# Kernel tuning notes

Measured on AMD Instinct MI355X. Metric: run time of the kernel, lower is better.

Reference implementation:

```python
import jax, jax.numpy as jnp
import numpy as np

NUM_CLASSES = 200
MARGIN = 0.6
LAMBDA_WEIGHT = 0.2
ALPHA = 1.5
GAMMA = 0.8
EPS = 1e-8


def setup_inputs() -> dict:
    key = jax.random.key(0)
    k1, k2 = jax.random.split(key)
    B, D = 32768, 512
    features = jax.random.normal(k1, (B, D), dtype=jnp.float32)
    labels = jax.random.randint(k2, (B,), 0, NUM_CLASSES, dtype=jnp.int64)
    return {"features": features, "labels": labels}


def reference(features, labels):
    B, D = features.shape
    C = NUM_CLASSES
    labels = labels.astype(jnp.int32)

    # Per-class prototypes (segment mean), matching mask-sum / (count + eps)
    proto_sum = jax.ops.segment_sum(features, labels, num_segments=C)      # [C, D]
    counts = jax.ops.segment_sum(jnp.ones((B,), features.dtype), labels, num_segments=C)
    prototypes = proto_sum / (counts[:, None] + EPS)                       # [C, D]

    # Squared distances from every sample to every prototype via Gram trick
    f2 = jnp.sum(features * features, axis=1, keepdims=True)               # [B, 1]
    p2 = jnp.sum(prototypes * prototypes, axis=1)                          # [C]
    d2 = jnp.maximum(f2 + p2[None, :] - 2.0 * features @ prototypes.T, 0.0)  # [B, C]

    # Nearest negative prototype: mask out the positive class with +inf
    pos_mask = jnp.arange(C)[None, :] == labels[:, None]                   # [B, C]
    neg_idx = jnp.argmin(jnp.where(pos_mask, jnp.inf, d2), axis=1)         # [B]

    # Exact squared distances to positive / chosen negative prototypes
    pos_proto = prototypes[labels]                                         # [B, D]
    neg_proto = prototypes[neg_idx]                                        # [B, D]
    d_ap = jnp.sum((features - pos_proto) ** 2, axis=1)                    # [B]
    d_an = jnp.sum((features - neg_proto) ** 2, axis=1)                    # [B]

    # Replicate the original's sequential normalization (d_ap is updated first)
    d_ap_n = d_ap / (d_ap + d_an + EPS)
    d_an_n = d_an / (d_ap_n + d_an + EPS)

    per_sample = jnp.maximum(0.0, ALPHA * d_ap_n - GAMMA * d_an_n + MARGIN)
    contrastive_loss = jnp.mean(per_sample)
    return jnp.abs(LAMBDA_WEIGHT * contrastive_loss)
```

## Files before the change

kernel.cpp:

```cpp
#include <hip/hip_runtime.h>
#include <hip/hip_bf16.h>

#define NCLS 200
#define NPADP 224
#define NTW 7
#define DIM 512
#define NSAMP 32768
#define NSEG 8
#define CAP 32
#define BM 64
#define BK 32
#define KIT 16
#define BSTR 40

typedef __attribute__((ext_vector_type(4))) float f32x4;
typedef __attribute__((ext_vector_type(4))) int   i32x4;
typedef __attribute__((ext_vector_type(8))) short bf16x8;

__device__ inline short bf16s(float x) {
  __hip_bfloat16 h = __float2bfloat16(x);
  return *reinterpret_cast<short*>(&h);
}

__device__ inline bf16x8 pack8(f32x4 a, f32x4 b) {
  bf16x8 r;
  r[0] = bf16s(a[0]); r[1] = bf16s(a[1]); r[2] = bf16s(a[2]); r[3] = bf16s(a[3]);
  r[4] = bf16s(b[0]); r[5] = bf16s(b[1]); r[6] = bf16s(b[2]); r[7] = bf16s(b[3]);
  return r;
}

__device__ inline float sumsq(f32x4 a) {
  return a[0]*a[0] + a[1]*a[1] + a[2]*a[2] + a[3]*a[3];
}

__device__ inline void bar_lgkm() {
  asm volatile("s_waitcnt lgkmcnt(0)" ::: "memory");
  __builtin_amdgcn_s_barrier();
}

__global__ __launch_bounds__(512) void k_psum(
    const float* __restrict__ feat, const int* __restrict__ labels,
    float* __restrict__ psum, int* __restrict__ pcnt)
{
  const int bx = blockIdx.x;
  const int c = bx >> 3, s = bx & 7;
  const int tid = threadIdx.x;
  const int lane = tid & 63;
  const int w = tid >> 6;

  __shared__ int   lists[8][CAP];
  __shared__ int   cnts[8];
  __shared__ float partial[8][DIM];

  int cnt = 0;
  const int segbase = s * (NSAMP / NSEG) + w * (NSAMP / NSEG / 8);
  #pragma unroll
  for (int i = 0; i < 2; ++i) {
    const int base = segbase + i * 256 + lane * 4;
    const i32x4 lab4 = *(const i32x4*)(labels + base);
    #pragma unroll
    for (int u = 0; u < 4; ++u) {
      const bool m = (lab4[u] == c);
      const unsigned long long bal = __ballot(m);
      if (m) {
        const int pos = cnt + __popcll(bal & ((1ull << lane) - 1ull));
        if (pos < CAP) lists[w][pos] = base + u;
      }
      cnt += __popcll(bal);
    }
  }
  if (cnt > CAP) cnt = CAP;
  if (lane == 0) cnts[w] = cnt;

  float aE[8], aO[8];
  #pragma unroll
  for (int q = 0; q < 8; ++q) { aE[q] = 0.f; aO[q] = 0.f; }
  int j = 0;
  for (; j + 2 <= cnt; j += 2) {
    const int r0 = lists[w][j], r1 = lists[w][j + 1];
    const f32x4 a0 = *(const f32x4*)(feat + (size_t)r0 * DIM + lane * 8);
    const f32x4 b0 = *(const f32x4*)(feat + (size_t)r0 * DIM + lane * 8 + 4);
    const f32x4 a1 = *(const f32x4*)(feat + (size_t)r1 * DIM + lane * 8);
    const f32x4 b1 = *(const f32x4*)(feat + (size_t)r1 * DIM + lane * 8 + 4);
    aE[0] += a0[0]; aE[1] += a0[1]; aE[2] += a0[2]; aE[3] += a0[3];
    aE[4] += b0[0]; aE[5] += b0[1]; aE[6] += b0[2]; aE[7] += b0[3];
    aO[0] += a1[0]; aO[1] += a1[1]; aO[2] += a1[2]; aO[3] += a1[3];
    aO[4] += b1[0]; aO[5] += b1[1]; aO[6] += b1[2]; aO[7] += b1[3];
  }
  if (j < cnt) {
    const int r0 = lists[w][j];
    const f32x4 a0 = *(const f32x4*)(feat + (size_t)r0 * DIM + lane * 8);
    const f32x4 b0 = *(const f32x4*)(feat + (size_t)r0 * DIM + lane * 8 + 4);
    aE[0] += a0[0]; aE[1] += a0[1]; aE[2] += a0[2]; aE[3] += a0[3];
    aE[4] += b0[0]; aE[5] += b0[1]; aE[6] += b0[2]; aE[7] += b0[3];
  }
  #pragma unroll
  for (int q = 0; q < 8; ++q) partial[w][lane * 8 + q] = aE[q] + aO[q];
  __syncthreads();

  int total = 0;
  #pragma unroll
  for (int u = 0; u < 8; ++u) total += cnts[u];
  float sv = 0.f;
  #pragma unroll
  for (int u = 0; u < 8; ++u) sv += partial[u][tid];
  psum[(size_t)(s * NCLS + c) * DIM + tid] = sv;
  if (tid == 0) pcnt[s * NCLS + c] = total;
}

__global__ __launch_bounds__(256) void k_pcomb(
    const float* __restrict__ psum, const int* __restrict__ pcnt,
    unsigned short* __restrict__ protoI, float* __restrict__ p2out)
{
  const int c = blockIdx.x;
  const int tid = threadIdx.x;
  const int d0 = tid, d1 = tid + 256;
  if (c >= NCLS) {
    protoI[((size_t)(d0 >> 5) * NPADP + c) * 32 + (d0 & 31)] = 0;
    protoI[((size_t)(d1 >> 5) * NPADP + c) * 32 + (d1 & 31)] = 0;
    if (tid == 0) p2out[c] = 1e30f;
    return;
  }
  __shared__ float red[256];
  float a0 = 0.f, a1 = 0.f;
  int total = 0;
  #pragma unroll
  for (int s = 0; s < NSEG; ++s) {
    a0 += psum[(size_t)(s * NCLS + c) * DIM + d0];
    a1 += psum[(size_t)(s * NCLS + c) * DIM + d1];
    total += pcnt[s * NCLS + c];
  }
  const float inv = 1.0f / ((float)total + 1e-8f);
  const float p0 = a0 * inv, p1 = a1 * inv;
  protoI[((size_t)(d0 >> 5) * NPADP + c) * 32 + (d0 & 31)] = (unsigned short)bf16s(p0);
  protoI[((size_t)(d1 >> 5) * NPADP + c) * 32 + (d1 & 31)] = (unsigned short)bf16s(p1);

  red[tid] = p0 * p0 + p1 * p1;
  __syncthreads();
  for (int st = 128; st > 0; st >>= 1) {
    if (tid < st) red[tid] += red[tid + st];
    __syncthreads();
  }
  if (tid == 0) p2out[c] = red[0];
}

__global__ __launch_bounds__(256, 2) void k_score(
    const float* __restrict__ feat, const int* __restrict__ labels,
    const unsigned short* __restrict__ protoI, const float* __restrict__ p2,
    float* __restrict__ partials)
{
  __shared__ __align__(16) unsigned short As[2][BM * BK];
  __shared__ __align__(16) unsigned short Bs[2][NPADP * BSTR];
  __shared__ float f2s[BM][4];
  __shared__ float rd_d[2][BM];
  __shared__ int   rd_c[2][BM];
  __shared__ float rd_p[2][BM];

  const int tid = threadIdx.x;
  const int lane = tid & 63;
  const int w = tid >> 6;
  const int wm = w >> 1, wn = w & 1;
  const int lr = lane & 15;
  const int kg = lane >> 4;
  const int blockRow = blockIdx.x * BM;

  const int arow = tid >> 2, apart = tid & 3;
  const float* agp = feat + (size_t)(blockRow + arow) * DIM + apart * 8;
  const int aoff = arow * BK + ((apart ^ (arow & 3)) * 8);
  const int brow = tid;

#define ISSUE(T, A0, A1, B0, B1, B2, B3) do {                                   \
    const float* ag_ = agp + (T) * BK;                                          \
    A0 = *(const f32x4*)(ag_);                                                  \
    A1 = *(const f32x4*)(ag_ + 4);                                              \
    if (brow < NPADP) {                                                         \
      const f32x4* bg_ = (const f32x4*)(protoI + ((size_t)(T) * NPADP + brow) * 32); \
      B0 = bg_[0]; B1 = bg_[1]; B2 = bg_[2]; B3 = bg_[3];                       \
    }                                                                           \
  } while (0)

#define STORE(NB, A0, A1, B0, B1, B2, B3) do {                                  \
    f2part += sumsq(A0) + sumsq(A1);                                            \
    *(bf16x8*)&As[NB][aoff] = pack8(A0, A1);                                    \
    if (brow < NPADP) {                                                         \
      *(f32x4*)&Bs[NB][brow * BSTR + 0]  = B0;                                  \
      *(f32x4*)&Bs[NB][brow * BSTR + 8]  = B1;                                  \
      *(f32x4*)&Bs[NB][brow * BSTR + 16] = B2;                                  \
      *(f32x4*)&Bs[NB][brow * BSTR + 24] = B3;                                  \
    }                                                                           \
  } while (0)

#define COMPUTE(CUR) do {                                                       \
    const bf16x8 Af0 = *(const bf16x8*)&As[CUR][ar0];                           \
    const bf16x8 Af1 = *(const bf16x8*)&As[CUR][ar1];                           \
    _Pragma("unroll")                                                           \
    for (int n = 0; n < NTW; ++n) {                                             \
      const bf16x8 Bf = *(const bf16x8*)&Bs[CUR][boff + n * (16 * BSTR)];       \
      acc0[n] = __builtin_amdgcn_mfma_f32_16x16x32_bf16(Af0, Bf, acc0[n], 0, 0, 0); \
      acc1[n] = __builtin_amdgcn_mfma_f32_16x16x32_bf16(Af1, Bf, acc1[n], 0, 0, 0); \
    }                                                                           \
  } while (0)

  float f2part = 0.f;
  f32x4 aA0, aA1, bA0, bA1, bA2, bA3;
  f32x4 aB0, aB1, bB0, bB1, bB2, bB3;

  ISSUE(0, aA0, aA1, bA0, bA1, bA2, bA3);
  STORE(0, aA0, aA1, bA0, bA1, bA2, bA3);
  ISSUE(1, aB0, aB1, bB0, bB1, bB2, bB3);
  bar_lgkm();

  f32x4 acc0[NTW], acc1[NTW];
  #pragma unroll
  for (int n = 0; n < NTW; ++n) {
    acc0[n] = f32x4{0.f, 0.f, 0.f, 0.f};
    acc1[n] = f32x4{0.f, 0.f, 0.f, 0.f};
  }

  const int r0v = wm * 32 + lr;
  const int r1v = r0v + 16;
  const int ar0 = r0v * BK + ((kg ^ (r0v & 3)) * 8);
  const int ar1 = r1v * BK + ((kg ^ (r1v & 3)) * 8);
  const int boff = (wn * (NTW * 16) + lr) * BSTR + kg * 8;

  #pragma unroll
  for (int p = 0; p < KIT / 2; ++p) {
    const int t0 = 2 * p, t1 = 2 * p + 1;
    COMPUTE(0);
    if (t0 + 2 < KIT) ISSUE(t0 + 2, aA0, aA1, bA0, bA1, bA2, bA3);
    STORE(1, aB0, aB1, bB0, bB1, bB2, bB3);
    bar_lgkm();
    COMPUTE(1);
    if (t1 + 2 < KIT) {
      ISSUE(t1 + 2, aB0, aB1, bB0, bB1, bB2, bB3);
      STORE(0, aA0, aA1, bA0, bA1, bA2, bA3);
      bar_lgkm();
    }
  }

  f2s[arow][apart] = f2part;
  __syncthreads();

  float p2v[NTW];
  #pragma unroll
  for (int n = 0; n < NTW; ++n) p2v[n] = p2[wn * (NTW * 16) + n * 16 + lr];

  #pragma unroll
  for (int m = 0; m < 2; ++m) {
    #pragma unroll
    for (int r = 0; r < 4; ++r) {
      const int srow = kg * 4 + r;
      const int lrow = wm * 32 + m * 16 + srow;
      const float f2v = (f2s[lrow][0] + f2s[lrow][1]) + (f2s[lrow][2] + f2s[lrow][3]);
      const int lab = labels[blockRow + lrow];
      float bestd = 1e38f; int bestc = 1 << 30;
      float posd = -1.f;
      #pragma unroll
      for (int n = 0; n < NTW; ++n) {
        const int cidx = wn * (NTW * 16) + n * 16 + lr;
        const float sc = (m == 0) ? acc0[n][r] : acc1[n][r];
        const float d2 = fmaxf(f2v + p2v[n] - 2.0f * sc, 0.0f);
        if (cidx == lab) posd = d2;
        else if (cidx < NCLS &&
                 (d2 < bestd || (d2 == bestd && cidx < bestc))) { bestd = d2; bestc = cidx; }
      }
      #pragma unroll
      for (int sft = 1; sft < 16; sft <<= 1) {
        const float od = __shfl_xor(bestd, sft);
        const int   oc = __shfl_xor(bestc, sft);
        const float op = __shfl_xor(posd, sft);
        if (od < bestd || (od == bestd && oc < bestc)) { bestd = od; bestc = oc; }
        posd = fmaxf(posd, op);
      }
      if (lr == 0) {
        rd_d[wn][lrow] = bestd; rd_c[wn][lrow] = bestc; rd_p[wn][lrow] = posd;
      }
    }
  }
  __syncthreads();

  if (tid < BM) {
    const float d0 = rd_d[0][tid], d1 = rd_d[1][tid];
    const int   c0 = rd_c[0][tid], c1 = rd_c[1][tid];
    float bestd; int bestc;
    if (d1 < d0 || (d1 == d0 && c1 < c0)) { bestd = d1; bestc = c1; }
    else                                  { bestd = d0; bestc = c0; }
    (void)bestc;
    const float posd = fmaxf(rd_p[0][tid], rd_p[1][tid]);
    const float dap = posd, dan = bestd;
    const float dapn = dap / (dap + dan + 1e-8f);
    const float dann = dan / (dapn + dan + 1e-8f);
    float v = fmaxf(0.f, 1.5f * dapn - 0.8f * dann + 0.6f);
    #pragma unroll
    for (int sft = 1; sft < 64; sft <<= 1) v += __shfl_xor(v, sft);
    if (tid == 0) partials[blockIdx.x] = v;
  }
#undef ISSUE
#undef STORE
#undef COMPUTE
}

__global__ __launch_bounds__(256) void k_finish(const float* __restrict__ partials,
                                                float* __restrict__ out)
{
  __shared__ float red[256];
  const int tid = threadIdx.x;
  red[tid] = partials[tid] + partials[tid + 256];
  __syncthreads();
  for (int st = 128; st > 0; st >>= 1) {
    if (tid < st) red[tid] += red[tid + st];
    __syncthreads();
  }
  if (tid == 0) out[0] = fabsf(0.2f * (red[0] / (float)NSAMP));
}

extern "C" void kernel_launch(void* const* d_in, const int* in_sizes, int n_in,
                              void* d_out, int out_size, void* d_ws, size_t ws_size,
                              hipStream_t stream) {
  const float* feat = (const float*)d_in[0];
  const int* labels = (const int*)d_in[1];
  float* out = (float*)d_out;

  char* ws = (char*)d_ws;
  unsigned short* protoI = (unsigned short*)ws;
  float* p2 = (float*)(ws + 229376);
  float* partials = (float*)(ws + 230400);
  float* psum = (float*)(ws + 232448);
  int* pcnt = (int*)(ws + 3509248);

  k_psum<<<NSEG * NCLS, 512, 0, stream>>>(feat, labels, psum, pcnt);
  k_pcomb<<<NPADP, 256, 0, stream>>>(psum, pcnt, protoI, p2);
  k_score<<<512, 256, 0, stream>>>(feat, labels, protoI, p2, partials);
  k_finish<<<1, 256, 0, stream>>>(partials, out);
}
```

Before: 46.63 us.

## Load A fragments directly to registers and stage prototypes in 128-wide K chunks

The scoring kernel no longer stages feature rows through shared memory. Each wave loads its A fragments straight from global memory into registers, converts them to bf16 in place, and computes squared norms with cross-lane shuffles. Prototypes are now stored row-major and staged into a single XOR-swizzled shared buffer, 128 K elements per pass, giving four passes instead of sixteen double-buffered steps. This cuts barriers and LDS traffic for A, but removes the double buffering, so global load latency for the prototype tile is less hidden and register pressure goes up.

```diff
diff --git a/kernel.cpp b/kernel.cpp
--- a/kernel.cpp
+++ b/kernel.cpp
@@ -9,9 +9,8 @@
 #define NSEG 8
 #define CAP 32
 #define BM 64
-#define BK 32
-#define KIT 16
-#define BSTR 40
+#define NPASS 4
+#define KQ 128
 
 typedef __attribute__((ext_vector_type(4))) float f32x4;
 typedef __attribute__((ext_vector_type(4))) int   i32x4;
@@ -110,14 +109,13 @@
 
 __global__ __launch_bounds__(256) void k_pcomb(
     const float* __restrict__ psum, const int* __restrict__ pcnt,
-    unsigned short* __restrict__ protoI, float* __restrict__ p2out)
+    unsigned short* __restrict__ protoB, float* __restrict__ p2out)
 {
   const int c = blockIdx.x;
   const int tid = threadIdx.x;
-  const int d0 = tid, d1 = tid + 256;
   if (c >= NCLS) {
-    protoI[((size_t)(d0 >> 5) * NPADP + c) * 32 + (d0 & 31)] = 0;
-    protoI[((size_t)(d1 >> 5) * NPADP + c) * 32 + (d1 & 31)] = 0;
+    protoB[(size_t)c * DIM + tid] = 0;
+    protoB[(size_t)c * DIM + 256 + tid] = 0;
     if (tid == 0) p2out[c] = 1e30f;
     return;
   }
@@ -126,14 +124,14 @@
   int total = 0;
   #pragma unroll
   for (int s = 0; s < NSEG; ++s) {
-    a0 += psum[(size_t)(s * NCLS + c) * DIM + d0];
-    a1 += psum[(size_t)(s * NCLS + c) * DIM + d1];
+    a0 += psum[(size_t)(s * NCLS + c) * DIM + tid];
+    a1 += psum[(size_t)(s * NCLS + c) * DIM + 256 + tid];
     total += pcnt[s * NCLS + c];
   }
   const float inv = 1.0f / ((float)total + 1e-8f);
   const float p0 = a0 * inv, p1 = a1 * inv;
-  protoI[((size_t)(d0 >> 5) * NPADP + c) * 32 + (d0 & 31)] = (unsigned short)bf16s(p0);
-  protoI[((size_t)(d1 >> 5) * NPADP + c) * 32 + (d1 & 31)] = (unsigned short)bf16s(p1);
+  protoB[(size_t)c * DIM + tid] = (unsigned short)bf16s(p0);
+  protoB[(size_t)c * DIM + 256 + tid] = (unsigned short)bf16s(p1);
 
   red[tid] = p0 * p0 + p1 * p1;
   __syncthreads();
@@ -146,12 +144,10 @@
 
 __global__ __launch_bounds__(256, 2) void k_score(
     const float* __restrict__ feat, const int* __restrict__ labels,
-    const unsigned short* __restrict__ protoI, const float* __restrict__ p2,
+    const unsigned short* __restrict__ protoB, const float* __restrict__ p2,
     float* __restrict__ partials)
 {
-  __shared__ __align__(16) unsigned short As[2][BM * BK];
-  __shared__ __align__(16) unsigned short Bs[2][NPADP * BSTR];
-  __shared__ float f2s[BM][4];
+  __shared__ __align__(16) unsigned short Bs[NPADP * KQ];
   __shared__ float rd_d[2][BM];
   __shared__ int   rd_c[2][BM];
   __shared__ float rd_p[2][BM];
@@ -164,51 +160,10 @@
   const int kg = lane >> 4;
   const int blockRow = blockIdx.x * BM;
 
-  const int arow = tid >> 2, apart = tid & 3;
-  const float* agp = feat + (size_t)(blockRow + arow) * DIM + apart * 8;
-  const int aoff = arow * BK + ((apart ^ (arow & 3)) * 8);
-  const int brow = tid;
-
-#define ISSUE(T, A0, A1, B0, B1, B2, B3) do {                                   \
-    const float* ag_ = agp + (T) * BK;                                          \
-    A0 = *(const f32x4*)(ag_);                                                  \
-    A1 = *(const f32x4*)(ag_ + 4);                                              \
-    if (brow < NPADP) {                                                         \
-      const f32x4* bg_ = (const f32x4*)(protoI + ((size_t)(T) * NPADP + brow) * 32); \
-      B0 = bg_[0]; B1 = bg_[1]; B2 = bg_[2]; B3 = bg_[3];                       \
-    }                                                                           \
-  } while (0)
-
-#define STORE(NB, A0, A1, B0, B1, B2, B3) do {                                  \
-    f2part += sumsq(A0) + sumsq(A1);                                            \
-    *(bf16x8*)&As[NB][aoff] = pack8(A0, A1);                                    \
-    if (brow < NPADP) {                                                         \
-      *(f32x4*)&Bs[NB][brow * BSTR + 0]  = B0;                                  \
-      *(f32x4*)&Bs[NB][brow * BSTR + 8]  = B1;                                  \
-      *(f32x4*)&Bs[NB][brow * BSTR + 16] = B2;                                  \
-      *(f32x4*)&Bs[NB][brow * BSTR + 24] = B3;                                  \
-    }                                                                           \
-  } while (0)
-
-#define COMPUTE(CUR) do {                                                       \
-    const bf16x8 Af0 = *(const bf16x8*)&As[CUR][ar0];                           \
-    const bf16x8 Af1 = *(const bf16x8*)&As[CUR][ar1];                           \
-    _Pragma("unroll")                                                           \
-    for (int n = 0; n < NTW; ++n) {                                             \
-      const bf16x8 Bf = *(const bf16x8*)&Bs[CUR][boff + n * (16 * BSTR)];       \
-      acc0[n] = __builtin_amdgcn_mfma_f32_16x16x32_bf16(Af0, Bf, acc0[n], 0, 0, 0); \
-      acc1[n] = __builtin_amdgcn_mfma_f32_16x16x32_bf16(Af1, Bf, acc1[n], 0, 0, 0); \
-    }                                                                           \
-  } while (0)
-
-  float f2part = 0.f;
-  f32x4 aA0, aA1, bA0, bA1, bA2, bA3;
-  f32x4 aB0, aB1, bB0, bB1, bB2, bB3;
-
-  ISSUE(0, aA0, aA1, bA0, bA1, bA2, bA3);
-  STORE(0, aA0, aA1, bA0, bA1, bA2, bA3);
-  ISSUE(1, aB0, aB1, bB0, bB1, bB2, bB3);
-  bar_lgkm();
+  const int r0v = wm * 32 + lr;
+  const int r1v = r0v + 16;
+  const float* a0p = feat + (size_t)(blockRow + r0v) * DIM;
+  const float* a1p = feat + (size_t)(blockRow + r1v) * DIM;
 
   f32x4 acc0[NTW], acc1[NTW];
   #pragma unroll
@@ -216,34 +171,72 @@
     acc0[n] = f32x4{0.f, 0.f, 0.f, 0.f};
     acc1[n] = f32x4{0.f, 0.f, 0.f, 0.f};
   }
-
-  const int r0v = wm * 32 + lr;
-  const int r1v = r0v + 16;
-  const int ar0 = r0v * BK + ((kg ^ (r0v & 3)) * 8);
-  const int ar1 = r1v * BK + ((kg ^ (r1v & 3)) * 8);
-  const int boff = (wn * (NTW * 16) + lr) * BSTR + kg * 8;
-
-  #pragma unroll
-  for (int p = 0; p < KIT / 2; ++p) {
-    const int t0 = 2 * p, t1 = 2 * p + 1;
-    COMPUTE(0);
-    if (t0 + 2 < KIT) ISSUE(t0 + 2, aA0, aA1, bA0, bA1, bA2, bA3);
-    STORE(1, aB0, aB1, bB0, bB1, bB2, bB3);
+  float f2a = 0.f, f2b = 0.f;
+
+#define ASTEP(X0, X1, X2, X3)                                                    \
+  do {                                                                           \
+    f2a += sumsq(X0) + sumsq(X1);                                                \
+    f2b += sumsq(X2) + sumsq(X3);                                                \
+    const bf16x8 Af0 = pack8(X0, X1);                                            \
+    const bf16x8 Af1 = pack8(X2, X3);                                            \
+    _Pragma("unroll")                                                            \
+    for (int n = 0; n < NTW; ++n) {                                              \
+      const int row = wn * 112 + n * 16 + lr;                                    \
+      const bf16x8 Bf = *(const bf16x8*)&Bs[row * KQ + (ulog ^ lr) * 8];         \
+      acc0[n] = __builtin_amdgcn_mfma_f32_16x16x32_bf16(Af0, Bf, acc0[n], 0, 0, 0); \
+      acc1[n] = __builtin_amdgcn_mfma_f32_16x16x32_bf16(Af1, Bf, acc1[n], 0, 0, 0); \
+    }                                                                            \
+  } while (0)
+
+  for (int p = 0; p < NPASS; ++p) {
+    f32x4 bst[14];
+    #pragma unroll
+    for (int i = 0; i < 14; ++i) {
+      const int u = i * 256 + tid;
+      const int row = u >> 4, uin = u & 15;
+      bst[i] = *(const f32x4*)(protoB + (size_t)row * DIM + p * KQ + uin * 8);
+    }
+    f32x4 aP0[8];
+    #pragma unroll
+    for (int s = 0; s < 2; ++s) {
+      const int ko = p * KQ + s * 32 + kg * 8;
+      aP0[s * 4 + 0] = *(const f32x4*)(a0p + ko);
+      aP0[s * 4 + 1] = *(const f32x4*)(a0p + ko + 4);
+      aP0[s * 4 + 2] = *(const f32x4*)(a1p + ko);
+      aP0[s * 4 + 3] = *(const f32x4*)(a1p + ko + 4);
+    }
     bar_lgkm();
-    COMPUTE(1);
-    if (t1 + 2 < KIT) {
-      ISSUE(t1 + 2, aB0, aB1, bB0, bB1, bB2, bB3);
-      STORE(0, aA0, aA1, bA0, bA1, bA2, bA3);
-      bar_lgkm();
-    }
-  }
-
-  f2s[arow][apart] = f2part;
-  __syncthreads();
+    #pragma unroll
+    for (int i = 0; i < 14; ++i) {
+      const int u = i * 256 + tid;
+      const int row = u >> 4, uin = u & 15;
+      *(f32x4*)&Bs[row * KQ + ((uin ^ (row & 15)) * 8)] = bst[i];
+    }
+    bar_lgkm();
+    f32x4 aP1[8];
+    #pragma unroll
+    for (int s = 0; s < 2; ++s) {
+      const int ko = p * KQ + (s + 2) * 32 + kg * 8;
+      aP1[s * 4 + 0] = *(const f32x4*)(a0p + ko);
+      aP1[s * 4 + 1] = *(const f32x4*)(a0p + ko + 4);
+      aP1[s * 4 + 2] = *(const f32x4*)(a1p + ko);
+      aP1[s * 4 + 3] = *(const f32x4*)(a1p + ko + 4);
+    }
+    {
+      { const int ulog = 0 * 4 + kg; ASTEP(aP0[0], aP0[1], aP0[2], aP0[3]); }
+      { const int ulog = 1 * 4 + kg; ASTEP(aP0[4], aP0[5], aP0[6], aP0[7]); }
+      { const int ulog = 2 * 4 + kg; ASTEP(aP1[0], aP1[1], aP1[2], aP1[3]); }
+      { const int ulog = 3 * 4 + kg; ASTEP(aP1[4], aP1[5], aP1[6], aP1[7]); }
+    }
+  }
+#undef ASTEP
+
+  f2a += __shfl_xor(f2a, 16); f2a += __shfl_xor(f2a, 32);
+  f2b += __shfl_xor(f2b, 16); f2b += __shfl_xor(f2b, 32);
 
   float p2v[NTW];
   #pragma unroll
-  for (int n = 0; n < NTW; ++n) p2v[n] = p2[wn * (NTW * 16) + n * 16 + lr];
+  for (int n = 0; n < NTW; ++n) p2v[n] = p2[wn * 112 + n * 16 + lr];
 
   #pragma unroll
   for (int m = 0; m < 2; ++m) {
@@ -251,13 +244,13 @@
     for (int r = 0; r < 4; ++r) {
       const int srow = kg * 4 + r;
       const int lrow = wm * 32 + m * 16 + srow;
-      const float f2v = (f2s[lrow][0] + f2s[lrow][1]) + (f2s[lrow][2] + f2s[lrow][3]);
+      const float f2v = __shfl(m == 0 ? f2a : f2b, srow);
       const int lab = labels[blockRow + lrow];
       float bestd = 1e38f; int bestc = 1 << 30;
       float posd = -1.f;
       #pragma unroll
       for (int n = 0; n < NTW; ++n) {
-        const int cidx = wn * (NTW * 16) + n * 16 + lr;
+        const int cidx = wn * 112 + n * 16 + lr;
         const float sc = (m == 0) ? acc0[n][r] : acc1[n][r];
         const float d2 = fmaxf(f2v + p2v[n] - 2.0f * sc, 0.0f);
         if (cidx == lab) posd = d2;
@@ -282,10 +275,9 @@
   if (tid < BM) {
     const float d0 = rd_d[0][tid], d1 = rd_d[1][tid];
     const int   c0 = rd_c[0][tid], c1 = rd_c[1][tid];
-    float bestd; int bestc;
-    if (d1 < d0 || (d1 == d0 && c1 < c0)) { bestd = d1; bestc = c1; }
-    else                                  { bestd = d0; bestc = c0; }
-    (void)bestc;
+    float bestd;
+    if (d1 < d0 || (d1 == d0 && c1 < c0)) bestd = d1;
+    else                                  bestd = d0;
     const float posd = fmaxf(rd_p[0][tid], rd_p[1][tid]);
     const float dap = posd, dan = bestd;
     const float dapn = dap / (dap + dan + 1e-8f);
@@ -295,9 +287,6 @@
     for (int sft = 1; sft < 64; sft <<= 1) v += __shfl_xor(v, sft);
     if (tid == 0) partials[blockIdx.x] = v;
   }
-#undef ISSUE
-#undef STORE
-#undef COMPUTE
 }
 
 __global__ __launch_bounds__(256) void k_finish(const float* __restrict__ partials,
@@ -322,14 +311,14 @@
   float* out = (float*)d_out;
 
   char* ws = (char*)d_ws;
-  unsigned short* protoI = (unsigned short*)ws;
+  unsigned short* protoB = (unsigned short*)ws;
   float* p2 = (float*)(ws + 229376);
   float* partials = (float*)(ws + 230400);
   float* psum = (float*)(ws + 232448);
   int* pcnt = (int*)(ws + 3509248);
 
   k_psum<<<NSEG * NCLS, 512, 0, stream>>>(feat, labels, psum, pcnt);
-  k_pcomb<<<NPADP, 256, 0, stream>>>(psum, pcnt, protoI, p2);
-  k_score<<<512, 256, 0, stream>>>(feat, labels, protoI, p2, partials);
+  k_pcomb<<<NPADP, 256, 0, stream>>>(psum, pcnt, protoB, p2);
+  k_score<<<512, 256, 0, stream>>>(feat, labels, protoB, p2, partials);
   k_finish<<<1, 256, 0, stream>>>(partials, out);
 }
```

Measured after the change: 53.03 us. 13.7% more time.

## Load A operands directly into registers, bypassing LDS staging

Applied to the files above, without the earlier changes.

The feature tile no longer passes through shared memory. Each wave loads its own MFMA A-fragments from global memory straight into registers, prefetching four k-steps ahead, and converts them to bf16 in place. The row squared norms are accumulated per lane and combined with shuffles instead of an LDS table and a block barrier. This removes the LDS writes and reads for A and one __syncthreads. In exchange, the two column-half waves each load the same feature rows (duplicate global loads), and the deeper prefetch raises register pressure, which may hurt occupancy at 2 blocks per SIMD.

```diff
diff --git a/kernel.cpp b/kernel.cpp
--- a/kernel.cpp
+++ b/kernel.cpp
@@ -9,7 +9,6 @@
 #define NSEG 8
 #define CAP 32
 #define BM 64
-#define BK 32
 #define KIT 16
 #define BSTR 40
 
@@ -149,9 +148,7 @@
     const unsigned short* __restrict__ protoI, const float* __restrict__ p2,
     float* __restrict__ partials)
 {
-  __shared__ __align__(16) unsigned short As[2][BM * BK];
   __shared__ __align__(16) unsigned short Bs[2][NPADP * BSTR];
-  __shared__ float f2s[BM][4];
   __shared__ float rd_d[2][BM];
   __shared__ int   rd_c[2][BM];
   __shared__ float rd_p[2][BM];
@@ -164,35 +161,49 @@
   const int kg = lane >> 4;
   const int blockRow = blockIdx.x * BM;
 
-  const int arow = tid >> 2, apart = tid & 3;
-  const float* agp = feat + (size_t)(blockRow + arow) * DIM + apart * 8;
-  const int aoff = arow * BK + ((apart ^ (arow & 3)) * 8);
+  const int r0v = wm * 32 + lr;
+  const float* a0p = feat + (size_t)(blockRow + r0v) * DIM;
+  const float* a1p = a0p + 16 * DIM;
   const int brow = tid;
 
-#define ISSUE(T, A0, A1, B0, B1, B2, B3) do {                                   \
-    const float* ag_ = agp + (T) * BK;                                          \
-    A0 = *(const f32x4*)(ag_);                                                  \
-    A1 = *(const f32x4*)(ag_ + 4);                                              \
+  f32x4 acc0[NTW], acc1[NTW];
+  #pragma unroll
+  for (int n = 0; n < NTW; ++n) {
+    acc0[n] = f32x4{0.f, 0.f, 0.f, 0.f};
+    acc1[n] = f32x4{0.f, 0.f, 0.f, 0.f};
+  }
+  float f2a = 0.f, f2b = 0.f;
+  const int boff = (wn * 112 + lr) * BSTR + kg * 8;
+
+#define ISSUE_A(T, S) do {                                                      \
+    const int ko_ = (T) * 32 + kg * 8;                                          \
+    S##0 = *(const f32x4*)(a0p + ko_);                                          \
+    S##1 = *(const f32x4*)(a0p + ko_ + 4);                                      \
+    S##2 = *(const f32x4*)(a1p + ko_);                                          \
+    S##3 = *(const f32x4*)(a1p + ko_ + 4);                                      \
+  } while (0)
+
+#define ISSUE_B(T, S) do {                                                      \
     if (brow < NPADP) {                                                         \
       const f32x4* bg_ = (const f32x4*)(protoI + ((size_t)(T) * NPADP + brow) * 32); \
-      B0 = bg_[0]; B1 = bg_[1]; B2 = bg_[2]; B3 = bg_[3];                       \
+      S##0 = bg_[0]; S##1 = bg_[1]; S##2 = bg_[2]; S##3 = bg_[3];               \
     }                                                                           \
   } while (0)
 
-#define STORE(NB, A0, A1, B0, B1, B2, B3) do {                                  \
-    f2part += sumsq(A0) + sumsq(A1);                                            \
-    *(bf16x8*)&As[NB][aoff] = pack8(A0, A1);                                    \
+#define STOREB(NB, S) do {                                                      \
     if (brow < NPADP) {                                                         \
-      *(f32x4*)&Bs[NB][brow * BSTR + 0]  = B0;                                  \
-      *(f32x4*)&Bs[NB][brow * BSTR + 8]  = B1;                                  \
-      *(f32x4*)&Bs[NB][brow * BSTR + 16] = B2;                                  \
-      *(f32x4*)&Bs[NB][brow * BSTR + 24] = B3;                                  \
+      *(f32x4*)&Bs[NB][brow * BSTR + 0]  = S##0;                                \
+      *(f32x4*)&Bs[NB][brow * BSTR + 8]  = S##1;                                \
+      *(f32x4*)&Bs[NB][brow * BSTR + 16] = S##2;                                \
+      *(f32x4*)&Bs[NB][brow * BSTR + 24] = S##3;                                \
     }                                                                           \
   } while (0)
 
-#define COMPUTE(CUR) do {                                                       \
-    const bf16x8 Af0 = *(const bf16x8*)&As[CUR][ar0];                           \
-    const bf16x8 Af1 = *(const bf16x8*)&As[CUR][ar1];                           \
+#define COMPUTE(CUR, S) do {                                                    \
+    f2a += sumsq(S##0) + sumsq(S##1);                                           \
+    f2b += sumsq(S##2) + sumsq(S##3);                                           \
+    const bf16x8 Af0 = pack8(S##0, S##1);                                       \
+    const bf16x8 Af1 = pack8(S##2, S##3);                                       \
     _Pragma("unroll")                                                           \
     for (int n = 0; n < NTW; ++n) {                                             \
       const bf16x8 Bf = *(const bf16x8*)&Bs[CUR][boff + n * (16 * BSTR)];       \
@@ -201,49 +212,59 @@
     }                                                                           \
   } while (0)
 
-  float f2part = 0.f;
-  f32x4 aA0, aA1, bA0, bA1, bA2, bA3;
-  f32x4 aB0, aB1, bB0, bB1, bB2, bB3;
-
-  ISSUE(0, aA0, aA1, bA0, bA1, bA2, bA3);
-  STORE(0, aA0, aA1, bA0, bA1, bA2, bA3);
-  ISSUE(1, aB0, aB1, bB0, bB1, bB2, bB3);
+  f32x4 A0_0, A0_1, A0_2, A0_3;
+  f32x4 A1_0, A1_1, A1_2, A1_3;
+  f32x4 A2_0, A2_1, A2_2, A2_3;
+  f32x4 A3_0, A3_1, A3_2, A3_3;
+  f32x4 bE_0, bE_1, bE_2, bE_3;
+  f32x4 bO_0, bO_1, bO_2, bO_3;
+
+  ISSUE_B(0, bE_);
+  ISSUE_A(0, A0_);
+  ISSUE_A(1, A1_);
+  ISSUE_A(2, A2_);
+  ISSUE_A(3, A3_);
+  STOREB(0, bE_);
+  ISSUE_B(1, bO_);
   bar_lgkm();
 
-  f32x4 acc0[NTW], acc1[NTW];
-  #pragma unroll
-  for (int n = 0; n < NTW; ++n) {
-    acc0[n] = f32x4{0.f, 0.f, 0.f, 0.f};
-    acc1[n] = f32x4{0.f, 0.f, 0.f, 0.f};
-  }
-
-  const int r0v = wm * 32 + lr;
-  const int r1v = r0v + 16;
-  const int ar0 = r0v * BK + ((kg ^ (r0v & 3)) * 8);
-  const int ar1 = r1v * BK + ((kg ^ (r1v & 3)) * 8);
-  const int boff = (wn * (NTW * 16) + lr) * BSTR + kg * 8;
-
-  #pragma unroll
-  for (int p = 0; p < KIT / 2; ++p) {
-    const int t0 = 2 * p, t1 = 2 * p + 1;
-    COMPUTE(0);
-    if (t0 + 2 < KIT) ISSUE(t0 + 2, aA0, aA1, bA0, bA1, bA2, bA3);
-    STORE(1, aB0, aB1, bB0, bB1, bB2, bB3);
+  #pragma unroll
+  for (int p = 0; p < 4; ++p) {
+    const int c = 4 * p;
+    COMPUTE(0, A0_);
+    if (c + 4 < KIT) ISSUE_A(c + 4, A0_);
+    ISSUE_B(c + 2, bE_);
+    STOREB(1, bO_);
     bar_lgkm();
-    COMPUTE(1);
-    if (t1 + 2 < KIT) {
-      ISSUE(t1 + 2, aB0, aB1, bB0, bB1, bB2, bB3);
-      STORE(0, aA0, aA1, bA0, bA1, bA2, bA3);
+    COMPUTE(1, A1_);
+    if (c + 5 < KIT) ISSUE_A(c + 5, A1_);
+    ISSUE_B(c + 3, bO_);
+    STOREB(0, bE_);
+    bar_lgkm();
+    COMPUTE(0, A2_);
+    if (c + 6 < KIT) ISSUE_A(c + 6, A2_);
+    if (c + 4 < KIT) ISSUE_B(c + 4, bE_);
+    STOREB(1, bO_);
+    bar_lgkm();
+    COMPUTE(1, A3_);
+    if (c + 7 < KIT) ISSUE_A(c + 7, A3_);
+    if (c + 5 < KIT) ISSUE_B(c + 5, bO_);
+    if (c + 4 < KIT) {
+      STOREB(0, bE_);
       bar_lgkm();
     }
   }
-
-  f2s[arow][apart] = f2part;
-  __syncthreads();
+#undef ISSUE_A
+#undef ISSUE_B
+#undef STOREB
+#undef COMPUTE
+
+  f2a += __shfl_xor(f2a, 16); f2a += __shfl_xor(f2a, 32);
+  f2b += __shfl_xor(f2b, 16); f2b += __shfl_xor(f2b, 32);
 
   float p2v[NTW];
   #pragma unroll
-  for (int n = 0; n < NTW; ++n) p2v[n] = p2[wn * (NTW * 16) + n * 16 + lr];
+  for (int n = 0; n < NTW; ++n) p2v[n] = p2[wn * 112 + n * 16 + lr];
 
   #pragma unroll
   for (int m = 0; m < 2; ++m) {
@@ -251,13 +272,13 @@
     for (int r = 0; r < 4; ++r) {
       const int srow = kg * 4 + r;
       const int lrow = wm * 32 + m * 16 + srow;
-      const float f2v = (f2s[lrow][0] + f2s[lrow][1]) + (f2s[lrow][2] + f2s[lrow][3]);
+      const float f2v = __shfl(m == 0 ? f2a : f2b, srow);
       const int lab = labels[blockRow + lrow];
       float bestd = 1e38f; int bestc = 1 << 30;
       float posd = -1.f;
       #pragma unroll
       for (int n = 0; n < NTW; ++n) {
-        const int cidx = wn * (NTW * 16) + n * 16 + lr;
+        const int cidx = wn * 112 + n * 16 + lr;
         const float sc = (m == 0) ? acc0[n][r] : acc1[n][r];
         const float d2 = fmaxf(f2v + p2v[n] - 2.0f * sc, 0.0f);
         if (cidx == lab) posd = d2;
@@ -282,10 +303,9 @@
   if (tid < BM) {
     const float d0 = rd_d[0][tid], d1 = rd_d[1][tid];
     const int   c0 = rd_c[0][tid], c1 = rd_c[1][tid];
-    float bestd; int bestc;
-    if (d1 < d0 || (d1 == d0 && c1 < c0)) { bestd = d1; bestc = c1; }
-    else                                  { bestd = d0; bestc = c0; }
-    (void)bestc;
+    float bestd;
+    if (d1 < d0 || (d1 == d0 && c1 < c0)) bestd = d1;
+    else                                  bestd = d0;
     const float posd = fmaxf(rd_p[0][tid], rd_p[1][tid]);
     const float dap = posd, dan = bestd;
     const float dapn = dap / (dap + dan + 1e-8f);
@@ -295,9 +315,6 @@
     for (int sft = 1; sft < 64; sft <<= 1) v += __shfl_xor(v, sft);
     if (tid == 0) partials[blockIdx.x] = v;
   }
-#undef ISSUE
-#undef STORE
-#undef COMPUTE
 }
 
 __global__ __launch_bounds__(256) void k_finish(const float* __restrict__ partials,
```

Result: slower. 74.56 us (+59.9%).

## Stream prototype tiles straight into LDS with global_load_lds and XOR swizzle

Applied to the files above, without the earlier changes.

k_pcomb now writes the bf16 prototypes in a 256-row, XOR-swizzled chunk layout. k_score copies each B tile straight from global memory into LDS with global_load_lds, instead of staging it through registers into a padded-stride buffer. The main loop becomes a single-step double buffer with explicit vmcnt/lgkmcnt waits. The aim is to cut register pressure and VALU/LDS store work for the B operand and to overlap loads with MFMA, at the cost of larger LDS tiles, extra padding rows, and dropping the two-blocks-per-CU launch bound hint.

```diff
diff --git a/kernel.cpp b/kernel.cpp
--- a/kernel.cpp
+++ b/kernel.cpp
@@ -3,6 +3,7 @@
 
 #define NCLS 200
 #define NPADP 224
+#define NROWS 256
 #define NTW 7
 #define DIM 512
 #define NSAMP 32768
@@ -11,7 +12,7 @@
 #define BM 64
 #define BK 32
 #define KIT 16
-#define BSTR 40
+#define CHUS (NROWS*32)
 
 typedef __attribute__((ext_vector_type(4))) float f32x4;
 typedef __attribute__((ext_vector_type(4))) int   i32x4;
@@ -31,11 +32,6 @@
 
 __device__ inline float sumsq(f32x4 a) {
   return a[0]*a[0] + a[1]*a[1] + a[2]*a[2] + a[3]*a[3];
-}
-
-__device__ inline void bar_lgkm() {
-  asm volatile("s_waitcnt lgkmcnt(0)" ::: "memory");
-  __builtin_amdgcn_s_barrier();
 }
 
 __global__ __launch_bounds__(512) void k_psum(
@@ -114,10 +110,14 @@
 {
   const int c = blockIdx.x;
   const int tid = threadIdx.x;
-  const int d0 = tid, d1 = tid + 256;
+  const int sw = (c >> 1) & 3;
   if (c >= NCLS) {
-    protoI[((size_t)(d0 >> 5) * NPADP + c) * 32 + (d0 & 31)] = 0;
-    protoI[((size_t)(d1 >> 5) * NPADP + c) * 32 + (d1 & 31)] = 0;
+    #pragma unroll
+    for (int h = 0; h < 2; ++h) {
+      const int d = tid + h * 256;
+      const int ck = d >> 5, uL = (d >> 3) & 3, e = d & 7;
+      protoI[(size_t)ck * CHUS + c * 32 + (uL ^ sw) * 8 + e] = 0;
+    }
     if (tid == 0) p2out[c] = 1e30f;
     return;
   }
@@ -126,14 +126,22 @@
   int total = 0;
   #pragma unroll
   for (int s = 0; s < NSEG; ++s) {
-    a0 += psum[(size_t)(s * NCLS + c) * DIM + d0];
-    a1 += psum[(size_t)(s * NCLS + c) * DIM + d1];
+    a0 += psum[(size_t)(s * NCLS + c) * DIM + tid];
+    a1 += psum[(size_t)(s * NCLS + c) * DIM + 256 + tid];
     total += pcnt[s * NCLS + c];
   }
   const float inv = 1.0f / ((float)total + 1e-8f);
   const float p0 = a0 * inv, p1 = a1 * inv;
-  protoI[((size_t)(d0 >> 5) * NPADP + c) * 32 + (d0 & 31)] = (unsigned short)bf16s(p0);
-  protoI[((size_t)(d1 >> 5) * NPADP + c) * 32 + (d1 & 31)] = (unsigned short)bf16s(p1);
+  {
+    const int d = tid;
+    const int ck = d >> 5, uL = (d >> 3) & 3, e = d & 7;
+    protoI[(size_t)ck * CHUS + c * 32 + (uL ^ sw) * 8 + e] = (unsigned short)bf16s(p0);
+  }
+  {
+    const int d = tid + 256;
+    const int ck = d >> 5, uL = (d >> 3) & 3, e = d & 7;
+    protoI[(size_t)ck * CHUS + c * 32 + (uL ^ sw) * 8 + e] = (unsigned short)bf16s(p1);
+  }
 
   red[tid] = p0 * p0 + p1 * p1;
   __syncthreads();
@@ -144,13 +152,13 @@
   if (tid == 0) p2out[c] = red[0];
 }
 
-__global__ __launch_bounds__(256, 2) void k_score(
+__global__ __launch_bounds__(256) void k_score(
     const float* __restrict__ feat, const int* __restrict__ labels,
     const unsigned short* __restrict__ protoI, const float* __restrict__ p2,
     float* __restrict__ partials)
 {
   __shared__ __align__(16) unsigned short As[2][BM * BK];
-  __shared__ __align__(16) unsigned short Bs[2][NPADP * BSTR];
+  __shared__ __align__(1024) unsigned short Bs[2][CHUS];
   __shared__ float f2s[BM][4];
   __shared__ float rd_d[2][BM];
   __shared__ int   rd_c[2][BM];
@@ -167,26 +175,41 @@
   const int arow = tid >> 2, apart = tid & 3;
   const float* agp = feat + (size_t)(blockRow + arow) * DIM + apart * 8;
   const int aoff = arow * BK + ((apart ^ (arow & 3)) * 8);
-  const int brow = tid;
-
-#define ISSUE(T, A0, A1, B0, B1, B2, B3) do {                                   \
+
+  float f2part = 0.f;
+
+  f32x4 acc0[NTW], acc1[NTW];
+  #pragma unroll
+  for (int n = 0; n < NTW; ++n) {
+    acc0[n] = f32x4{0.f, 0.f, 0.f, 0.f};
+    acc1[n] = f32x4{0.f, 0.f, 0.f, 0.f};
+  }
+
+  const int r0v = wm * 32 + lr;
+  const int r1v = r0v + 16;
+  const int ar0 = r0v * BK + ((kg ^ (r0v & 3)) * 8);
+  const int ar1 = r1v * BK + ((kg ^ (r1v & 3)) * 8);
+
+#define ISSUE_A(T, S) do {                                                      \
     const float* ag_ = agp + (T) * BK;                                          \
-    A0 = *(const f32x4*)(ag_);                                                  \
-    A1 = *(const f32x4*)(ag_ + 4);                                              \
-    if (brow < NPADP) {                                                         \
-      const f32x4* bg_ = (const f32x4*)(protoI + ((size_t)(T) * NPADP + brow) * 32); \
-      B0 = bg_[0]; B1 = bg_[1]; B2 = bg_[2]; B3 = bg_[3];                       \
-    }                                                                           \
-  } while (0)
-
-#define STORE(NB, A0, A1, B0, B1, B2, B3) do {                                  \
-    f2part += sumsq(A0) + sumsq(A1);                                            \
-    *(bf16x8*)&As[NB][aoff] = pack8(A0, A1);                                    \
-    if (brow < NPADP) {                                                         \
-      *(f32x4*)&Bs[NB][brow * BSTR + 0]  = B0;                                  \
-      *(f32x4*)&Bs[NB][brow * BSTR + 8]  = B1;                                  \
-      *(f32x4*)&Bs[NB][brow * BSTR + 16] = B2;                                  \
-      *(f32x4*)&Bs[NB][brow * BSTR + 24] = B3;                                  \
+    S##0 = *(const f32x4*)(ag_);                                                \
+    S##1 = *(const f32x4*)(ag_ + 4);                                            \
+  } while (0)
+
+#define STOREA(NB, S) do {                                                      \
+    f2part += sumsq(S##0) + sumsq(S##1);                                        \
+    *(bf16x8*)&As[NB][aoff] = pack8(S##0, S##1);                                \
+  } while (0)
+
+#define BGLD(T, NB) do {                                                        \
+    _Pragma("unroll")                                                           \
+    for (int i_ = 0; i_ < 4; ++i_) {                                            \
+      const int j_ = w * 4 + i_;                                                \
+      const unsigned short* g_ = protoI + (size_t)(T) * CHUS + j_ * 512 + lane * 8; \
+      unsigned short* l_ = &Bs[NB][j_ * 512];                                   \
+      __builtin_amdgcn_global_load_lds(                                         \
+          (const __attribute__((address_space(1))) void*)g_,                    \
+          (__attribute__((address_space(3))) void*)l_, 16, 0, 0);               \
     }                                                                           \
   } while (0)
 
@@ -195,55 +218,65 @@
     const bf16x8 Af1 = *(const bf16x8*)&As[CUR][ar1];                           \
     _Pragma("unroll")                                                           \
     for (int n = 0; n < NTW; ++n) {                                             \
-      const bf16x8 Bf = *(const bf16x8*)&Bs[CUR][boff + n * (16 * BSTR)];       \
+      const int row_ = wn * 112 + n * 16 + lr;                                  \
+      const bf16x8 Bf = *(const bf16x8*)&Bs[CUR][row_ * 32 + ((kg ^ ((row_ >> 1) & 3)) * 8)]; \
       acc0[n] = __builtin_amdgcn_mfma_f32_16x16x32_bf16(Af0, Bf, acc0[n], 0, 0, 0); \
       acc1[n] = __builtin_amdgcn_mfma_f32_16x16x32_bf16(Af1, Bf, acc1[n], 0, 0, 0); \
     }                                                                           \
   } while (0)
 
-  float f2part = 0.f;
-  f32x4 aA0, aA1, bA0, bA1, bA2, bA3;
-  f32x4 aB0, aB1, bB0, bB1, bB2, bB3;
-
-  ISSUE(0, aA0, aA1, bA0, bA1, bA2, bA3);
-  STORE(0, aA0, aA1, bA0, bA1, bA2, bA3);
-  ISSUE(1, aB0, aB1, bB0, bB1, bB2, bB3);
-  bar_lgkm();
-
-  f32x4 acc0[NTW], acc1[NTW];
-  #pragma unroll
-  for (int n = 0; n < NTW; ++n) {
-    acc0[n] = f32x4{0.f, 0.f, 0.f, 0.f};
-    acc1[n] = f32x4{0.f, 0.f, 0.f, 0.f};
-  }
-
-  const int r0v = wm * 32 + lr;
-  const int r1v = r0v + 16;
-  const int ar0 = r0v * BK + ((kg ^ (r0v & 3)) * 8);
-  const int ar1 = r1v * BK + ((kg ^ (r1v & 3)) * 8);
-  const int boff = (wn * (NTW * 16) + lr) * BSTR + kg * 8;
-
-  #pragma unroll
-  for (int p = 0; p < KIT / 2; ++p) {
-    const int t0 = 2 * p, t1 = 2 * p + 1;
-    COMPUTE(0);
-    if (t0 + 2 < KIT) ISSUE(t0 + 2, aA0, aA1, bA0, bA1, bA2, bA3);
-    STORE(1, aB0, aB1, bB0, bB1, bB2, bB3);
-    bar_lgkm();
-    COMPUTE(1);
-    if (t1 + 2 < KIT) {
-      ISSUE(t1 + 2, aB0, aB1, bB0, bB1, bB2, bB3);
-      STORE(0, aA0, aA1, bA0, bA1, bA2, bA3);
-      bar_lgkm();
-    }
-  }
+#define BAR_VM2() do {                                                          \
+    asm volatile("s_waitcnt vmcnt(2)" ::: "memory");                            \
+    asm volatile("s_waitcnt lgkmcnt(0)" ::: "memory");                          \
+    __builtin_amdgcn_s_barrier();                                               \
+  } while (0)
+
+#define BAR_VM0() do {                                                          \
+    asm volatile("s_waitcnt vmcnt(0)" ::: "memory");                            \
+    asm volatile("s_waitcnt lgkmcnt(0)" ::: "memory");                          \
+    __builtin_amdgcn_s_barrier();                                               \
+  } while (0)
+
+  f32x4 AE_0, AE_1;
+  f32x4 AO_0, AO_1;
+
+  ISSUE_A(0, AE_);
+  BGLD(0, 0);
+  __builtin_amdgcn_sched_barrier(0);
+  ISSUE_A(1, AO_);
+  STOREA(0, AE_);
+  BAR_VM2();
+
+  #pragma unroll
+  for (int t = 0; t < KIT; ++t) {
+    const int cur = t & 1;
+    const int nxt = cur ^ 1;
+    if (t + 1 < KIT) {
+      if ((t & 1) == 0) STOREA(nxt, AO_); else STOREA(nxt, AE_);
+      BGLD(t + 1, nxt);
+      __builtin_amdgcn_sched_barrier(0);
+    }
+    if (t + 2 < KIT) {
+      if ((t & 1) == 0) ISSUE_A(t + 2, AE_); else ISSUE_A(t + 2, AO_);
+    }
+    COMPUTE(cur);
+    if (t + 1 < KIT) {
+      if (t + 2 < KIT) BAR_VM2(); else BAR_VM0();
+    }
+  }
+#undef ISSUE_A
+#undef STOREA
+#undef BGLD
+#undef COMPUTE
+#undef BAR_VM2
+#undef BAR_VM0
 
   f2s[arow][apart] = f2part;
   __syncthreads();
 
   float p2v[NTW];
   #pragma unroll
-  for (int n = 0; n < NTW; ++n) p2v[n] = p2[wn * (NTW * 16) + n * 16 + lr];
+  for (int n = 0; n < NTW; ++n) p2v[n] = p2[wn * 112 + n * 16 + lr];
 
   #pragma unroll
   for (int m = 0; m < 2; ++m) {
@@ -257,7 +290,7 @@
       float posd = -1.f;
       #pragma unroll
       for (int n = 0; n < NTW; ++n) {
-        const int cidx = wn * (NTW * 16) + n * 16 + lr;
+        const int cidx = wn * 112 + n * 16 + lr;
         const float sc = (m == 0) ? acc0[n][r] : acc1[n][r];
         const float d2 = fmaxf(f2v + p2v[n] - 2.0f * sc, 0.0f);
         if (cidx == lab) posd = d2;
@@ -282,10 +315,9 @@
   if (tid < BM) {
     const float d0 = rd_d[0][tid], d1 = rd_d[1][tid];
     const int   c0 = rd_c[0][tid], c1 = rd_c[1][tid];
-    float bestd; int bestc;
-    if (d1 < d0 || (d1 == d0 && c1 < c0)) { bestd = d1; bestc = c1; }
-    else                                  { bestd = d0; bestc = c0; }
-    (void)bestc;
+    float bestd;
+    if (d1 < d0 || (d1 == d0 && c1 < c0)) bestd = d1;
+    else                                  bestd = d0;
     const float posd = fmaxf(rd_p[0][tid], rd_p[1][tid]);
     const float dap = posd, dan = bestd;
     const float dapn = dap / (dap + dan + 1e-8f);
@@ -295,9 +327,6 @@
     for (int sft = 1; sft < 64; sft <<= 1) v += __shfl_xor(v, sft);
     if (tid == 0) partials[blockIdx.x] = v;
   }
-#undef ISSUE
-#undef STORE
-#undef COMPUTE
 }
 
 __global__ __launch_bounds__(256) void k_finish(const float* __restrict__ partials,
@@ -323,10 +352,10 @@
 
   char* ws = (char*)d_ws;
   unsigned short* protoI = (unsigned short*)ws;
-  float* p2 = (float*)(ws + 229376);
-  float* partials = (float*)(ws + 230400);
-  float* psum = (float*)(ws + 232448);
-  int* pcnt = (int*)(ws + 3509248);
+  float* p2 = (float*)(ws + 262144);
+  float* partials = (float*)(ws + 263168);
+  float* psum = (float*)(ws + 266240);
+  int* pcnt = (int*)(ws + 266240 + 3276800);
 
   k_psum<<<NSEG * NCLS, 512, 0, stream>>>(feat, labels, psum, pcnt);
   k_pcomb<<<NPADP, 256, 0, stream>>>(psum, pcnt, protoI, p2);
```

Result: no change. 46.09 us (-1.2%).
